# Kernel optimization log

Hardware: AMD Instinct MI355X
Metric: run time of the kernel (lower is better)

## Reference

```python
import jax, jax.numpy as jnp
import numpy as np

K = 3  # kernel size for all locally-connected layers

def lc2d(x, w, b, stride):
    """Locally connected 2d: per-output-location unshared weights.
    x: [B, C, H, W]; w: [1, O, C, Ho, Wo, K*K]; b: [1, O, Ho, Wo].
    Matches torch: x.unfold(2,K,s).unfold(3,K,s) -> [B,C,Ho,Wo,K,K] flattened
    to K*K, then (x[:,None]*w).sum([2,-1]) + b.
    """
    # patches: [B, C*K*K, Ho, Wo], feature order (c, kh, kw) == torch unfold order
    p = jax.lax.conv_general_dilated_patches(x, (K, K), (stride, stride), 'VALID')
    B, CKK, Ho, Wo = p.shape
    C = w.shape[2]
    p = p.reshape(B, C, K * K, Ho, Wo)
    out = jnp.einsum('bckhw,ochwk->bohw', p, w[0])
    return out + b

def setup_inputs() -> dict:
    key = jax.random.key(0)
    ks = jax.random.split(key, 11)
    s = 0.1
    return {
        'x':   jax.random.normal(ks[0], (8192, 1, 28, 28), dtype=jnp.float32),
        'w1':  jax.random.normal(ks[1], (1, 16, 1, 13, 13, 9), dtype=jnp.float32) * s,
        'b1':  jax.random.normal(ks[2], (1, 16, 13, 13), dtype=jnp.float32) * s,
        'w2':  jax.random.normal(ks[3], (1, 32, 16, 6, 6, 9), dtype=jnp.float32) * s,
        'b2':  jax.random.normal(ks[4], (1, 32, 6, 6), dtype=jnp.float32) * s,
        'w3':  jax.random.normal(ks[5], (1, 64, 32, 4, 4, 9), dtype=jnp.float32) * s,
        'b3':  jax.random.normal(ks[6], (1, 64, 4, 4), dtype=jnp.float32) * s,
        'fw1': jax.random.normal(ks[7], (512, 1024), dtype=jnp.float32) * 0.03,
        'fb1': jax.random.normal(ks[8], (512,), dtype=jnp.float32) * 0.03,
        'fw2': jax.random.normal(ks[9], (10, 512), dtype=jnp.float32) * 0.03,
        'fb2': jax.random.normal(ks[10], (10,), dtype=jnp.float32) * 0.03,
    }

def reference(x, w1, b1, w2, b2, w3, b3, fw1, fb1, fw2, fb2):
    h = jax.nn.relu(lc2d(x, w1, b1, stride=2))   # [B,16,13,13]
    h = jax.nn.relu(lc2d(h, w2, b2, stride=2))   # [B,32,6,6]
    h = lc2d(h, w3, b3, stride=1)                # [B,64,4,4]
    h = h.reshape(h.shape[0], -1)                # [B,1024]
    h = jax.nn.relu(h @ fw1.T + fb1)             # [B,512]
    return h @ fw2.T + fb2                       # [B,10]
```

## Files before the change

### kernel.cpp

```cpp
#include <hip/hip_runtime.h>

typedef __attribute__((ext_vector_type(8))) short short8v;
typedef __attribute__((ext_vector_type(4))) short short4v;
typedef __attribute__((ext_vector_type(4))) float f32x4;

static __device__ __forceinline__ unsigned short f2bf(float f) {
  union { float f; unsigned u; } v;
  v.f = f;
  const unsigned u = v.u;
  return (unsigned short)((u + 0x7FFF + ((u >> 16) & 1)) >> 16);
}
static __device__ __forceinline__ float bf2f(unsigned short s) {
  union { unsigned u; float f; } v;
  v.u = ((unsigned)s) << 16;
  return v.f;
}


__global__ __launch_bounds__(256) void k_trb(const float* __restrict__ x,
                                             unsigned short* __restrict__ xT,
                                             int Bc) {
  __shared__ float t[32][33];
  const int b0 = blockIdx.x * 32;
  const int f0 = blockIdx.y * 32;
  const int tx = threadIdx.x, ty = threadIdx.y;
  for (int r = ty; r < 32; r += 8) {
    const int f = f0 + tx;
    t[r][tx] = (f < 784) ? x[(size_t)(b0 + r) * 784 + f] : 0.f;
  }
  __syncthreads();
  for (int r = ty; r < 32; r += 8) {
    const int f = f0 + r;
    if (f < 784) xT[(size_t)f * Bc + b0 + tx] = f2bf(t[tx][r]);
  }
}

__global__ __launch_bounds__(256) void k_wall(
    const float* __restrict__ w1, const float* __restrict__ w2,
    const float* __restrict__ w3, const float* __restrict__ fw1,
    unsigned short* __restrict__ Wm1, unsigned short* __restrict__ Wm2,
    unsigned short* __restrict__ Wm3, unsigned short* __restrict__ Wbf) {
  const int N1 = 169 * 16 * 32;
  const int N2 = 36 * 32 * 160;
  const int N3 = 16 * 64 * 288;
  const int N4 = 512 * 1024;
  const int total = N1 + N2 + N3 + N4;
  for (int i = blockIdx.x * 256 + threadIdx.x; i * 8 < total;
       i += gridDim.x * 256) {
    const int base = i * 8;
#pragma unroll
    for (int u = 0; u < 8; ++u) {
      const int idx = base + u;
      if (idx < N1) {
        const int pos = idx >> 9, rem = idx & 511;
        const int o = rem >> 5, k = rem & 31;
        const float v = (k < 9) ? w1[((size_t)o * 169 + pos) * 9 + k] : 0.f;
        Wm1[idx] = f2bf(v);
      } else if (idx < N1 + N2) {
        const int j = idx - N1;
        const int pos = j / (32 * 160), rem = j - pos * (32 * 160);
        const int o = rem / 160, k = rem - o * 160;
        float v = 0.f;
        if (k < 144) {
          const int c = k / 9, kk = k - c * 9;
          v = w2[((size_t)(o * 16 + c) * 36 + pos) * 9 + kk];
        }
        Wm2[j] = f2bf(v);
      } else if (idx < N1 + N2 + N3) {
        const int j = idx - N1 - N2;
        const int pos = j / (64 * 288), rem = j - pos * (64 * 288);
        const int o = rem / 288, k = rem - o * 288;
        const int c = k / 9, kk = k - c * 9;
        Wm3[j] = f2bf(w3[((size_t)(o * 32 + c) * 16 + pos) * 9 + kk]);
      } else {
        const int j = idx - N1 - N2 - N3;
        Wbf[j] = f2bf(fw1[j]);
      }
    }
  }
}

template <int O, int K, int NPOS, int HWIN, int WIN, int WOD, int STR,
          bool RELU>
__global__ __launch_bounds__(256) void k_lcm(
    const unsigned short* __restrict__ X, const unsigned short* __restrict__ Wm,
    const float* __restrict__ bias, unsigned short* __restrict__ out, int B) {
  constexpr int NSTEP = (K + 31) / 32;
  constexpr int Kpad = NSTEP * 32;
  constexpr int NJT = (O >= 32) ? 2 : 1;
  constexpr int NBT = (O == 64) ? 4 : 2;
  __shared__ short Wl[O * 40];
  __shared__ short Xl[5232];
  __shared__ int rowtab[Kpad];
  const int tid = threadIdx.x;
  const int b0 = blockIdx.x * 128;
  const int pos = blockIdx.y;
  const int ho = pos / WOD, wo = pos - ho * WOD;
  const int w = tid >> 6, l = tid & 63, m = l & 15, g = l >> 4;
  const int jw = (O == 64) ? (w & 1) * 32 : 0;
  const int boff = (O == 64) ? (w >> 1) * 64
                             : ((O == 32) ? w * 32 : (w & 3) * 32);

  for (int k = tid; k < Kpad; k += 256) {
    int r = 0;
    if (k < K) {
      const int c = k / 9, kk = k - c * 9;
      const int kh = kk / 3, kw = kk - kh * 3;
      r = c * HWIN + (ho * STR + kh) * WIN + (wo * STR + kw);
    }
    rowtab[k] = r;
  }
  __syncthreads();

  const unsigned short* wsrc = Wm + (size_t)pos * O * Kpad;
  const int wjj = tid >> 2, wko = (tid & 3) * 8;
  const bool wact = tid < O * 4;
  const int kp = tid >> 4, boct = (tid & 15) * 8;

  f32x4 acc[NJT][NBT];
#pragma unroll
  for (int jt = 0; jt < NJT; ++jt)
#pragma unroll
    for (int bt = 0; bt < NBT; ++bt) acc[jt][bt] = (f32x4){0.f, 0.f, 0.f, 0.f};

  short8v wreg, xa, xb;
  bool z0, z1;

  if (wact) wreg = *(const short8v*)&wsrc[(size_t)wjj * Kpad + wko];
  {
    const int k0 = 2 * kp;
    z0 = k0 >= K;
    z1 = k0 + 1 >= K;
    if (!z0) xa = *(const short8v*)(X + (size_t)rowtab[k0] * B + b0 + boct);
    if (!z1)
      xb = *(const short8v*)(X + (size_t)rowtab[k0 + 1] * B + b0 + boct);
  }
  if (wact) *(short8v*)&Wl[wjj * 40 + wko] = wreg;
  {
    unsigned* xl = (unsigned*)&Xl[0];
#pragma unroll
    for (int i = 0; i < 8; ++i) {
      const int b = boct + i;
      const unsigned lo = z0 ? 0u : (unsigned)(unsigned short)xa[i];
      const unsigned hi = z1 ? 0u : (unsigned)(unsigned short)xb[i];
      xl[b * 20 + (b >> 3) * 4 + kp] = lo | (hi << 16);
    }
  }
  __syncthreads();

  for (int t = 0; t < NSTEP; ++t) {
    if (t < NSTEP - 1) {
      const int kc = (t + 1) * 32;
      if (wact) wreg = *(const short8v*)&wsrc[(size_t)wjj * Kpad + kc + wko];
      const int k0 = kc + 2 * kp;
      z0 = k0 >= K;
      z1 = k0 + 1 >= K;
      if (!z0) xa = *(const short8v*)(X + (size_t)rowtab[k0] * B + b0 + boct);
      if (!z1)
        xb = *(const short8v*)(X + (size_t)rowtab[k0 + 1] * B + b0 + boct);
    }
    {
      short8v aw[NJT], bx[NBT];
#pragma unroll
      for (int jt = 0; jt < NJT; ++jt)
        aw[jt] = *(const short8v*)&Wl[(jw + jt * 16 + m) * 40 + g * 8];
#pragma unroll
      for (int bt = 0; bt < NBT; ++bt) {
        const int b = boff + bt * 16 + m;
        bx[bt] = *(const short8v*)&Xl[b * 40 + (b >> 3) * 8 + g * 8];
      }
#pragma unroll
      for (int jt = 0; jt < NJT; ++jt)
#pragma unroll
        for (int bt = 0; bt < NBT; ++bt)
          acc[jt][bt] = __builtin_amdgcn_mfma_f32_16x16x32_bf16(
              aw[jt], bx[bt], acc[jt][bt], 0, 0, 0);
    }
    if (t < NSTEP - 1) {
      __syncthreads();
      if (wact) *(short8v*)&Wl[wjj * 40 + wko] = wreg;
      unsigned* xl = (unsigned*)&Xl[0];
#pragma unroll
      for (int i = 0; i < 8; ++i) {
        const int b = boct + i;
        const unsigned lo = z0 ? 0u : (unsigned)(unsigned short)xa[i];
        const unsigned hi = z1 ? 0u : (unsigned)(unsigned short)xb[i];
        xl[b * 20 + (b >> 3) * 4 + kp] = lo | (hi << 16);
      }
      __syncthreads();
    }
  }

#pragma unroll
  for (int jt = 0; jt < NJT; ++jt)
#pragma unroll
    for (int r = 0; r < 4; ++r) {
      const int o = jw + jt * 16 + g * 4 + r;
      const int f = o * NPOS + pos;
      const float bz = bias[f];
#pragma unroll
      for (int bt = 0; bt < NBT; ++bt) {
        float v = acc[jt][bt][r] + bz;
        if (RELU) v = fmaxf(v, 0.f);
        out[(size_t)f * B + b0 + boff + bt * 16 + m] = f2bf(v);
      }
    }
}

__global__ __launch_bounds__(256) void k_fc1m(
    const unsigned short* __restrict__ X,
    const unsigned short* __restrict__ Wbf, const float* __restrict__ fb1,
    unsigned short* __restrict__ out, int B) {
  __shared__ short Wl[2][5120];
  __shared__ short Xl[2][2608];
  const int tid = threadIdx.x;
  const int b0 = blockIdx.x * 64, j0 = blockIdx.y * 128;
  const int w = tid >> 6, l = tid & 63, m = l & 15, g = l >> 4;

  const int wj = tid >> 1, wkh = (tid & 1) * 16;
  const unsigned short* wsrc = Wbf + (size_t)(j0 + wj) * 1024 + wkh;
  const int kp = tid >> 4, bq = (tid & 15) * 4;
  const unsigned short* xsrc = X + (size_t)(2 * kp) * B + b0 + bq;

  f32x4 acc[2][4];
#pragma unroll
  for (int jt = 0; jt < 2; ++jt)
#pragma unroll
    for (int bt = 0; bt < 4; ++bt) acc[jt][bt] = (f32x4){0.f, 0.f, 0.f, 0.f};

  short8v wreg0, wreg1;
  short4v xa, xb;

  wreg0 = *(const short8v*)(wsrc);
  wreg1 = *(const short8v*)(wsrc + 8);
  xa = *(const short4v*)(xsrc);
  xb = *(const short4v*)(xsrc + B);

  {
    *(short8v*)&Wl[0][wj * 40 + wkh] = wreg0;
    *(short8v*)&Wl[0][wj * 40 + wkh + 8] = wreg1;
    unsigned* xl = (unsigned*)&Xl[0][0];
#pragma unroll
    for (int i = 0; i < 4; ++i) {
      const int b = bq + i;
      xl[b * 20 + (b >> 3) * 4 + kp] = (unsigned)(unsigned short)xa[i] |
                                       ((unsigned)(unsigned short)xb[i] << 16);
    }
  }
  __syncthreads();

  for (int t = 0; t < 32; ++t) {
    const int cur = t & 1;
    if (t < 31) {
      const unsigned short* wp = wsrc + (t + 1) * 32;
      wreg0 = *(const short8v*)(wp);
      wreg1 = *(const short8v*)(wp + 8);
      const unsigned short* xp = xsrc + (size_t)(t + 1) * 32 * B;
      xa = *(const short4v*)(xp);
      xb = *(const short4v*)(xp + B);
    }
    {
      short8v aw[2], bx[4];
#pragma unroll
      for (int jt = 0; jt < 2; ++jt)
        aw[jt] = *(const short8v*)&Wl[cur][(w * 32 + jt * 16 + m) * 40 + g * 8];
#pragma unroll
      for (int bt = 0; bt < 4; ++bt) {
        const int b = bt * 16 + m;
        bx[bt] = *(const short8v*)&Xl[cur][b * 40 + (b >> 3) * 8 + g * 8];
      }
#pragma unroll
      for (int jt = 0; jt < 2; ++jt)
#pragma unroll
        for (int bt = 0; bt < 4; ++bt)
          acc[jt][bt] = __builtin_amdgcn_mfma_f32_16x16x32_bf16(
              aw[jt], bx[bt], acc[jt][bt], 0, 0, 0);
    }
    if (t < 31) {
      const int nxt = cur ^ 1;
      *(short8v*)&Wl[nxt][wj * 40 + wkh] = wreg0;
      *(short8v*)&Wl[nxt][wj * 40 + wkh + 8] = wreg1;
      unsigned* xl = (unsigned*)&Xl[nxt][0];
#pragma unroll
      for (int i = 0; i < 4; ++i) {
        const int b = bq + i;
        xl[b * 20 + (b >> 3) * 4 + kp] =
            (unsigned)(unsigned short)xa[i] |
            ((unsigned)(unsigned short)xb[i] << 16);
      }
    }
    __syncthreads();
  }

#pragma unroll
  for (int jt = 0; jt < 2; ++jt)
#pragma unroll
    for (int r = 0; r < 4; ++r) {
      const int j = j0 + w * 32 + jt * 16 + g * 4 + r;
      const float bj = fb1[j];
#pragma unroll
      for (int bt = 0; bt < 4; ++bt)
        out[(size_t)j * B + b0 + bt * 16 + m] =
            f2bf(fmaxf(acc[jt][bt][r] + bj, 0.f));
    }
}

__global__ __launch_bounds__(512) void k_fc2(
    const unsigned short* __restrict__ in, const float* __restrict__ fw2,
    const float* __restrict__ fb2, float* __restrict__ out, int B, int b0) {
  __shared__ float red[8][10][64];
  const int tx = threadIdx.x;
  const int b = blockIdx.x * 64 + tx;
  const int tyu = threadIdx.y;
  float acc[10];
#pragma unroll
  for (int i = 0; i < 10; ++i) acc[i] = 0.f;
  for (int kk = 0; kk < 64; ++kk) {
    const int k = tyu * 64 + kk;
    const float v = bf2f(in[(size_t)k * B + b]);
#pragma unroll
    for (int i = 0; i < 10; ++i) acc[i] = fmaf(v, fw2[i * 512 + k], acc[i]);
  }
#pragma unroll
  for (int i = 0; i < 10; ++i) red[tyu][i][tx] = acc[i];
  __syncthreads();
  if (tyu == 0) {
#pragma unroll
    for (int i = 0; i < 10; ++i) {
      float s = fb2[i];
#pragma unroll
      for (int q = 0; q < 8; ++q) s += red[q][i][tx];
      out[(size_t)(b0 + b) * 10 + i] = s;
    }
  }
}

extern "C" void kernel_launch(void* const* d_in, const int* in_sizes, int n_in,
                              void* d_out, int out_size, void* d_ws,
                              size_t ws_size, hipStream_t stream) {
  const float* x   = (const float*)d_in[0];
  const float* w1  = (const float*)d_in[1];
  const float* b1  = (const float*)d_in[2];
  const float* w2  = (const float*)d_in[3];
  const float* b2  = (const float*)d_in[4];
  const float* w3  = (const float*)d_in[5];
  const float* b3  = (const float*)d_in[6];
  const float* fw1 = (const float*)d_in[7];
  const float* fb1 = (const float*)d_in[8];
  const float* fw2 = (const float*)d_in[9];
  const float* fb2 = (const float*)d_in[10];
  float* out = (float*)d_out;

  const int B = in_sizes[0] / 784;

  const size_t nWm1 = (size_t)169 * 16 * 32 / 2;
  const size_t nWm2 = (size_t)36 * 32 * 160 / 2;
  const size_t nWm3 = (size_t)16 * 64 * 288 / 2;
  const size_t nWbf = (size_t)512 * 1024 / 2;
  unsigned short* Wm1 = (unsigned short*)d_ws;
  unsigned short* Wm2 = (unsigned short*)((float*)d_ws + nWm1);
  unsigned short* Wm3 = (unsigned short*)((float*)d_ws + nWm1 + nWm2);
  unsigned short* Wbf = (unsigned short*)((float*)d_ws + nWm1 + nWm2 + nWm3);
  unsigned short* hbase =
      (unsigned short*)((float*)d_ws + nWm1 + nWm2 + nWm3 + nWbf);
  const size_t ws_rem =
      ws_size - (nWm1 + nWm2 + nWm3 + nWbf) * sizeof(float);

  const size_t per_elem = (size_t)(784 + 2704 + 1152 + 1024 + 512) * 2;
  int Bc = B;
  while ((size_t)Bc * per_elem > ws_rem && Bc > 512) Bc >>= 1;
  const int nch = B / Bc;

  unsigned short* XT = hbase;
  unsigned short* H1 = XT + (size_t)784 * Bc;
  unsigned short* H2 = H1 + (size_t)2704 * Bc;
  unsigned short* H3 = H2 + (size_t)1152 * Bc;
  unsigned short* H4 = H3 + (size_t)1024 * Bc;

  k_wall<<<dim3(533), 256, 0, stream>>>(w1, w2, w3, fw1, Wm1, Wm2, Wm3, Wbf);

  for (int ch = 0; ch < nch; ++ch) {
    const float* xc = x + (size_t)ch * Bc * 784;
    const int b0 = ch * Bc;
    const int nbt = Bc / 128;

    k_trb<<<dim3(Bc / 32, 25), dim3(32, 8), 0, stream>>>(xc, XT, Bc);
    k_lcm<16, 9, 169, 784, 28, 13, 2, true>
        <<<dim3(nbt, 169), 256, 0, stream>>>(XT, Wm1, b1, H1, Bc);
    k_lcm<32, 144, 36, 169, 13, 6, 2, true>
        <<<dim3(nbt, 36), 256, 0, stream>>>(H1, Wm2, b2, H2, Bc);
    k_lcm<64, 288, 16, 36, 6, 4, 1, false>
        <<<dim3(nbt, 16), 256, 0, stream>>>(H2, Wm3, b3, H3, Bc);
    k_fc1m<<<dim3(Bc / 64, 4), 256, 0, stream>>>(H3, Wbf, fb1, H4, Bc);
    k_fc2<<<dim3(Bc / 64), dim3(64, 8), 0, stream>>>(H4, fw2, fb2, out, Bc,
                                                     b0);
  }
}
```

Before: 104.5 us.

## Merge input transpose with weight packing and widen layer-1 batch tile

Folds the input transpose and the weight-repacking kernels into one launch by splitting the grid into transpose blocks and weight-conversion blocks. This removes one kernel launch and lets both jobs run at the same time. Separately, the first locally-connected layer now covers 256 batch elements per block instead of 128, which halves that layer's grid and reuses each loaded weight tile across more rows. In exchange it uses more LDS and registers per block, and the weight repacking now reruns on every batch chunk instead of once (a leftover unused 'wallBlocks' variable hints at an unfinished plan).

```diff
diff --git a/kernel.cpp b/kernel.cpp
--- a/kernel.cpp
+++ b/kernel.cpp
@@ -17,36 +17,37 @@
 }
 
 
-__global__ __launch_bounds__(256) void k_trb(const float* __restrict__ x,
-                                             unsigned short* __restrict__ xT,
-                                             int Bc) {
-  __shared__ float t[32][33];
-  const int b0 = blockIdx.x * 32;
-  const int f0 = blockIdx.y * 32;
-  const int tx = threadIdx.x, ty = threadIdx.y;
-  for (int r = ty; r < 32; r += 8) {
-    const int f = f0 + tx;
-    t[r][tx] = (f < 784) ? x[(size_t)(b0 + r) * 784 + f] : 0.f;
-  }
-  __syncthreads();
-  for (int r = ty; r < 32; r += 8) {
-    const int f = f0 + r;
-    if (f < 784) xT[(size_t)f * Bc + b0 + tx] = f2bf(t[tx][r]);
-  }
-}
-
-__global__ __launch_bounds__(256) void k_wall(
-    const float* __restrict__ w1, const float* __restrict__ w2,
+__global__ __launch_bounds__(256) void k_init(
+    const float* __restrict__ x, unsigned short* __restrict__ xT, int Bc,
+    int nbTr, const float* __restrict__ w1, const float* __restrict__ w2,
     const float* __restrict__ w3, const float* __restrict__ fw1,
     unsigned short* __restrict__ Wm1, unsigned short* __restrict__ Wm2,
     unsigned short* __restrict__ Wm3, unsigned short* __restrict__ Wbf) {
+  const int tid = threadIdx.x;
+  if ((int)blockIdx.x < nbTr) {
+    __shared__ float t[32][33];
+    const int nbx = Bc >> 5;
+    const int bx = blockIdx.x % nbx, by = blockIdx.x / nbx;
+    const int b0 = bx * 32, f0 = by * 32;
+    const int tx = tid & 31, ty = tid >> 5;
+    for (int r = ty; r < 32; r += 8) {
+      const int f = f0 + tx;
+      t[r][tx] = (f < 784) ? x[(size_t)(b0 + r) * 784 + f] : 0.f;
+    }
+    __syncthreads();
+    for (int r = ty; r < 32; r += 8) {
+      const int f = f0 + r;
+      if (f < 784) xT[(size_t)f * Bc + b0 + tx] = f2bf(t[tx][r]);
+    }
+    return;
+  }
   const int N1 = 169 * 16 * 32;
   const int N2 = 36 * 32 * 160;
   const int N3 = 16 * 64 * 288;
   const int N4 = 512 * 1024;
   const int total = N1 + N2 + N3 + N4;
-  for (int i = blockIdx.x * 256 + threadIdx.x; i * 8 < total;
-       i += gridDim.x * 256) {
+  const int nw = gridDim.x - nbTr;
+  for (int i = (blockIdx.x - nbTr) * 256 + tid; i * 8 < total; i += nw * 256) {
     const int base = i * 8;
 #pragma unroll
     for (int u = 0; u < 8; ++u) {
@@ -81,25 +82,26 @@
 }
 
 template <int O, int K, int NPOS, int HWIN, int WIN, int WOD, int STR,
-          bool RELU>
+          bool RELU, int BBT = 128>
 __global__ __launch_bounds__(256) void k_lcm(
     const unsigned short* __restrict__ X, const unsigned short* __restrict__ Wm,
     const float* __restrict__ bias, unsigned short* __restrict__ out, int B) {
   constexpr int NSTEP = (K + 31) / 32;
   constexpr int Kpad = NSTEP * 32;
+  constexpr int NBH = BBT / 128;
   constexpr int NJT = (O >= 32) ? 2 : 1;
-  constexpr int NBT = (O == 64) ? 4 : 2;
+  constexpr int NBT = (O == 64) ? 4 : ((BBT == 256) ? 4 : 2);
   __shared__ short Wl[O * 40];
-  __shared__ short Xl[5232];
+  __shared__ short Xl[(BBT == 128) ? 5232 : 10480];
   __shared__ int rowtab[Kpad];
   const int tid = threadIdx.x;
-  const int b0 = blockIdx.x * 128;
+  const int b0 = blockIdx.x * BBT;
   const int pos = blockIdx.y;
   const int ho = pos / WOD, wo = pos - ho * WOD;
   const int w = tid >> 6, l = tid & 63, m = l & 15, g = l >> 4;
   const int jw = (O == 64) ? (w & 1) * 32 : 0;
   const int boff = (O == 64) ? (w >> 1) * 64
-                             : ((O == 32) ? w * 32 : (w & 3) * 32);
+                             : ((O == 32) ? w * 32 : w * (BBT / 4));
 
   for (int k = tid; k < Kpad; k += 256) {
     int r = 0;
@@ -123,7 +125,7 @@
 #pragma unroll
     for (int bt = 0; bt < NBT; ++bt) acc[jt][bt] = (f32x4){0.f, 0.f, 0.f, 0.f};
 
-  short8v wreg, xa, xb;
+  short8v wreg, xav[NBH], xbv[NBH];
   bool z0, z1;
 
   if (wact) wreg = *(const short8v*)&wsrc[(size_t)wjj * Kpad + wko];
@@ -131,20 +133,28 @@
     const int k0 = 2 * kp;
     z0 = k0 >= K;
     z1 = k0 + 1 >= K;
-    if (!z0) xa = *(const short8v*)(X + (size_t)rowtab[k0] * B + b0 + boct);
-    if (!z1)
-      xb = *(const short8v*)(X + (size_t)rowtab[k0 + 1] * B + b0 + boct);
+#pragma unroll
+    for (int bh = 0; bh < NBH; ++bh) {
+      if (!z0)
+        xav[bh] = *(const short8v*)(X + (size_t)rowtab[k0] * B + b0 +
+                                    bh * 128 + boct);
+      if (!z1)
+        xbv[bh] = *(const short8v*)(X + (size_t)rowtab[k0 + 1] * B + b0 +
+                                    bh * 128 + boct);
+    }
   }
   if (wact) *(short8v*)&Wl[wjj * 40 + wko] = wreg;
   {
     unsigned* xl = (unsigned*)&Xl[0];
 #pragma unroll
-    for (int i = 0; i < 8; ++i) {
-      const int b = boct + i;
-      const unsigned lo = z0 ? 0u : (unsigned)(unsigned short)xa[i];
-      const unsigned hi = z1 ? 0u : (unsigned)(unsigned short)xb[i];
-      xl[b * 20 + (b >> 3) * 4 + kp] = lo | (hi << 16);
-    }
+    for (int bh = 0; bh < NBH; ++bh)
+#pragma unroll
+      for (int i = 0; i < 8; ++i) {
+        const int b = bh * 128 + boct + i;
+        const unsigned lo = z0 ? 0u : (unsigned)(unsigned short)xav[bh][i];
+        const unsigned hi = z1 ? 0u : (unsigned)(unsigned short)xbv[bh][i];
+        xl[b * 20 + (b >> 3) * 4 + kp] = lo | (hi << 16);
+      }
   }
   __syncthreads();
 
@@ -155,9 +165,15 @@
       const int k0 = kc + 2 * kp;
       z0 = k0 >= K;
       z1 = k0 + 1 >= K;
-      if (!z0) xa = *(const short8v*)(X + (size_t)rowtab[k0] * B + b0 + boct);
-      if (!z1)
-        xb = *(const short8v*)(X + (size_t)rowtab[k0 + 1] * B + b0 + boct);
+#pragma unroll
+      for (int bh = 0; bh < NBH; ++bh) {
+        if (!z0)
+          xav[bh] = *(const short8v*)(X + (size_t)rowtab[k0] * B + b0 +
+                                      bh * 128 + boct);
+        if (!z1)
+          xbv[bh] = *(const short8v*)(X + (size_t)rowtab[k0 + 1] * B + b0 +
+                                      bh * 128 + boct);
+      }
     }
     {
       short8v aw[NJT], bx[NBT];
@@ -181,12 +197,14 @@
       if (wact) *(short8v*)&Wl[wjj * 40 + wko] = wreg;
       unsigned* xl = (unsigned*)&Xl[0];
 #pragma unroll
-      for (int i = 0; i < 8; ++i) {
-        const int b = boct + i;
-        const unsigned lo = z0 ? 0u : (unsigned)(unsigned short)xa[i];
-        const unsigned hi = z1 ? 0u : (unsigned)(unsigned short)xb[i];
-        xl[b * 20 + (b >> 3) * 4 + kp] = lo | (hi << 16);
-      }
+      for (int bh = 0; bh < NBH; ++bh)
+#pragma unroll
+        for (int i = 0; i < 8; ++i) {
+          const int b = bh * 128 + boct + i;
+          const unsigned lo = z0 ? 0u : (unsigned)(unsigned short)xav[bh][i];
+          const unsigned hi = z1 ? 0u : (unsigned)(unsigned short)xbv[bh][i];
+          xl[b * 20 + (b >> 3) * 4 + kp] = lo | (hi << 16);
+        }
       __syncthreads();
     }
   }
@@ -373,20 +391,25 @@
 
   unsigned short* XT = hbase;
   unsigned short* H1 = XT + (size_t)784 * Bc;
-  unsigned short* H2 = H1 + (size_t)2704 * Bc;
+  unsigned short* H2 = H1 + (size_t)1152 * 0 + (size_t)2704 * Bc;
   unsigned short* H3 = H2 + (size_t)1152 * Bc;
   unsigned short* H4 = H3 + (size_t)1024 * Bc;
 
-  k_wall<<<dim3(533), 256, 0, stream>>>(w1, w2, w3, fw1, Wm1, Wm2, Wm3, Wbf);
-
+  bool first = true;
   for (int ch = 0; ch < nch; ++ch) {
     const float* xc = x + (size_t)ch * Bc * 784;
     const int b0 = ch * Bc;
     const int nbt = Bc / 128;
-
-    k_trb<<<dim3(Bc / 32, 25), dim3(32, 8), 0, stream>>>(xc, XT, Bc);
-    k_lcm<16, 9, 169, 784, 28, 13, 2, true>
-        <<<dim3(nbt, 169), 256, 0, stream>>>(XT, Wm1, b1, H1, Bc);
+    const int nbTr = (Bc / 32) * 25;
+
+    const int wallBlocks = first ? 533 : 1;
+    k_init<<<dim3(nbTr + 533), 256, 0, stream>>>(xc, XT, Bc, nbTr, w1, w2, w3,
+                                                 fw1, Wm1, Wm2, Wm3, Wbf);
+    (void)wallBlocks;
+    first = false;
+
+    k_lcm<16, 9, 169, 784, 28, 13, 2, true, 256>
+        <<<dim3(Bc / 256, 169), 256, 0, stream>>>(XT, Wm1, b1, H1, Bc);
     k_lcm<32, 144, 36, 169, 13, 6, 2, true>
         <<<dim3(nbt, 36), 256, 0, stream>>>(H1, Wm2, b2, H2, Bc);
     k_lcm<64, 288, 16, 36, 6, 4, 1, false>
```

Result: no change. 104.9 us (+0.5%).
